# Optimization experiments

Hardware: AMD Instinct MI355X
Metric: run time of the kernel (lower is better)

## Reference

```python
import jax, jax.numpy as jnp
import numpy as np

N_NODES = 100000
N_EDGES = 1000000
DIM = 128
N_RELS = 500
N_TIMES = 1000


def setup_inputs() -> dict:
    key = jax.random.key(0)
    ks = jax.random.split(key, 8)
    h = jax.random.normal(ks[0], (N_NODES, DIM), dtype=jnp.float32)
    edge_index = jax.random.randint(ks[1], (2, N_EDGES), 0, N_NODES, dtype=jnp.int64)
    edge_type = jax.random.randint(ks[2], (N_EDGES,), 0, N_RELS, dtype=jnp.int64)
    edge_time = jax.random.randint(ks[3], (N_EDGES,), 0, N_TIMES, dtype=jnp.int64)
    query_rel = 7
    rel_table = jax.random.normal(ks[4], (N_RELS, DIM), dtype=jnp.float32)
    time_table = jax.random.normal(ks[5], (N_TIMES, DIM), dtype=jnp.float32)
    # Linear weights stored as [in, out] so y = x @ W + b
    W1 = jax.random.normal(ks[6], (4 * DIM, DIM), dtype=jnp.float32) * (1.0 / np.sqrt(4 * DIM))
    b1 = jnp.zeros((DIM,), dtype=jnp.float32)
    W2 = jax.random.normal(ks[7], (DIM, 1), dtype=jnp.float32) * (1.0 / np.sqrt(DIM))
    b2 = jnp.zeros((1,), dtype=jnp.float32)
    return {"h": h, "edge_index": edge_index, "edge_type": edge_type,
            "edge_time": edge_time, "query_rel": query_rel,
            "rel_table": rel_table, "time_table": time_table,
            "W1": W1, "b1": b1, "W2": W2, "b2": b2}


def reference(h, edge_index, edge_type, edge_time, query_rel,
              rel_table, time_table, W1, b1, W2, b2):
    src = edge_index[0]                    # [E]
    h_s = h[src]                           # [E, D] gather
    h_r = rel_table[edge_type]             # [E, D] embedding lookup
    h_t = time_table[edge_time]            # [E, D] embedding lookup
    h_rq = jnp.broadcast_to(rel_table[query_rel][None, :], h_s.shape)  # [E, D]
    x = jnp.concatenate([h_s, h_r, h_rq, h_t], axis=1)  # [E, 4D]
    hidden = jax.nn.relu(x @ W1 + b1)      # [E, D]
    alpha = hidden @ W2 + b2               # [E, 1]
    return jax.nn.sigmoid(alpha)[:, 0]     # [E]
```

## Files before the change

kernel.cpp:

```cpp
#include <hip/hip_runtime.h>
#include <hip/hip_fp16.h>
#include <hip/hip_fp8.h>
#include <math.h>

#define DIM 128

typedef _Float16 half8 __attribute__((ext_vector_type(8)));
typedef _Float16 half2v __attribute__((ext_vector_type(2)));
typedef float floatx4 __attribute__((ext_vector_type(4)));


__global__ __launch_bounds__(256) void precompute(
    const float* __restrict__ h, const float* __restrict__ rel,
    const float* __restrict__ tim, const int* __restrict__ qrel,
    const float* __restrict__ W1, const float* __restrict__ b1,
    unsigned char* __restrict__ H8, __half* __restrict__ Rh, __half* __restrict__ Th,
    int n_nodes, int n_rels, int n_times, int nHB, int nRB)
{
    const int tid = threadIdx.x;
    const int b = blockIdx.x;

    const float* A; int M, k0, row0; bool isR = false, isH = false;
    __half* Out = nullptr;
    if (b < nHB)            { A = h;   isH = true; M = n_nodes; k0 = 0;   row0 = b * 128; }
    else if (b < nHB + nRB) { A = rel; Out = Rh;   M = n_rels;  k0 = 128; row0 = (b - nHB) * 128; isR = true; }
    else                    { A = tim; Out = Th;   M = n_times; k0 = 384; row0 = (b - nHB - nRB) * 128; }

    __shared__ _Float16 fragB[32 * 64 * 8];
    __shared__ float c0f[DIM];

#pragma unroll
    for (int it = 0; it < 8; ++it) {
        const int o = tid + it * 256;
        const int ctkc = o >> 6, L = o & 63;
        const int ct = ctkc >> 2, kc = ctkc & 3;
        const int q = L >> 4, n15 = L & 15;
        const float* base = W1 + (size_t)(k0 + kc * 32 + q * 8) * DIM + ct * 16 + n15;
        half8 f;
#pragma unroll
        for (int j = 0; j < 8; ++j) f[j] = (_Float16)base[(size_t)j * DIM];
        *(half8*)&fragB[o * 8] = f;
    }
    if (isR && tid < DIM) {
        const int q = qrel[0];
        const float* hq = rel + (size_t)q * DIM;
        float s = b1[tid];
        for (int k = 0; k < DIM; ++k)
            s = fmaf(hq[k], W1[(size_t)(256 + k) * DIM + tid], s);
        c0f[tid] = s;
    }
    __syncthreads();

    const int w = tid >> 6;
    const int lane = tid & 63;
    const int m15 = lane & 15, q = lane >> 4;

    const float* aBase[2];
#pragma unroll
    for (int mt = 0; mt < 2; ++mt) {
        int arow = row0 + w * 32 + mt * 16 + m15;
        if (arow >= M) arow = M - 1;
        aBase[mt] = A + (size_t)arow * DIM + q * 8;
    }

    floatx4 acc[2][8];
#pragma unroll
    for (int mt = 0; mt < 2; ++mt)
#pragma unroll
        for (int ct = 0; ct < 8; ++ct) acc[mt][ct] = (floatx4)0.f;

#pragma unroll
    for (int kc = 0; kc < 4; ++kc) {
        half8 af[2];
#pragma unroll
        for (int mt = 0; mt < 2; ++mt) {
            const float4 a0 = *(const float4*)(aBase[mt] + kc * 32);
            const float4 a1 = *(const float4*)(aBase[mt] + kc * 32 + 4);
            af[mt][0] = (_Float16)a0.x; af[mt][1] = (_Float16)a0.y;
            af[mt][2] = (_Float16)a0.z; af[mt][3] = (_Float16)a0.w;
            af[mt][4] = (_Float16)a1.x; af[mt][5] = (_Float16)a1.y;
            af[mt][6] = (_Float16)a1.z; af[mt][7] = (_Float16)a1.w;
        }
#pragma unroll
        for (int ct = 0; ct < 8; ++ct) {
            const half8 bf = *(half8*)&fragB[(((ct * 4 + kc) * 64) + lane) * 8];
            acc[0][ct] = __builtin_amdgcn_mfma_f32_16x16x32_f16(af[0], bf, acc[0][ct], 0, 0, 0);
            acc[1][ct] = __builtin_amdgcn_mfma_f32_16x16x32_f16(af[1], bf, acc[1][ct], 0, 0, 0);
        }
    }

    float cadd[8];
#pragma unroll
    for (int ct = 0; ct < 8; ++ct) cadd[ct] = isR ? c0f[ct * 16 + m15] : 0.f;

#pragma unroll
    for (int mt = 0; mt < 2; ++mt)
#pragma unroll
        for (int r = 0; r < 4; ++r) {
            const int m = row0 + w * 32 + mt * 16 + q * 4 + r;
            if (m < M) {
                if (isH) {
                    uint2 pk;
#if __has_builtin(__builtin_amdgcn_cvt_pk_fp8_f32)
                    int w0 = 0, w1 = 0;
                    w0 = __builtin_amdgcn_cvt_pk_fp8_f32(acc[mt][0][r], acc[mt][1][r], w0, false);
                    w0 = __builtin_amdgcn_cvt_pk_fp8_f32(acc[mt][2][r], acc[mt][3][r], w0, true);
                    w1 = __builtin_amdgcn_cvt_pk_fp8_f32(acc[mt][4][r], acc[mt][5][r], w1, false);
                    w1 = __builtin_amdgcn_cvt_pk_fp8_f32(acc[mt][6][r], acc[mt][7][r], w1, true);
                    pk.x = (unsigned)w0; pk.y = (unsigned)w1;
#else
                    union { uint2 u; unsigned char bb[8]; } pu;
#pragma unroll
                    for (int ct = 0; ct < 8; ++ct)
                        pu.bb[ct] = __hip_fp8_e4m3(acc[mt][ct][r]).__x;
                    pk = pu.u;
#endif
                    *(uint2*)(H8 + (size_t)m * DIM + m15 * 8) = pk;
                } else {
                    half8 hv;
#pragma unroll
                    for (int ct = 0; ct < 8; ++ct)
                        hv[ct] = (_Float16)(acc[mt][ct][r] + cadd[ct]);
                    *(half8*)(Out + (size_t)m * DIM + m15 * 8) = hv;
                }
            }
        }
}

__device__ __forceinline__ half2v fp8x2_to_h2(unsigned u16) {
#if __has_builtin(__builtin_amdgcn_cvt_pk_f16_fp8)
    auto c = __builtin_amdgcn_cvt_pk_f16_fp8((short)u16);
    half2v r; r[0] = c[0]; r[1] = c[1];
    return r;
#else
    auto f = __builtin_amdgcn_cvt_pk_f32_fp8((int)u16, false);
    half2v r; r[0] = (_Float16)f[0]; r[1] = (_Float16)f[1];
    return r;
#endif
}

__device__ __forceinline__ float edot(uint2 hu, uint4 ru, uint4 tu,
                                      const half2v* __restrict__ w2h) {
    union U { uint4 u; half2v h[4]; };
    U R, T; R.u = ru; T.u = tu;
    const half2v z = (half2v)(_Float16)0.f;
    const unsigned hw[4] = {hu.x & 0xffffu, hu.x >> 16, hu.y & 0xffffu, hu.y >> 16};
    float p = 0.f;
#pragma unroll
    for (int j = 0; j < 4; ++j) {
        const half2v hh = fp8x2_to_h2(hw[j]);
        half2v s = hh + R.h[j] + T.h[j];
        s = __builtin_elementwise_max(s, z);
#if __has_builtin(__builtin_amdgcn_fdot2)
        p = __builtin_amdgcn_fdot2(s, w2h[j], p, false);
#else
        p = fmaf((float)s[0], (float)w2h[j][0], p);
        p = fmaf((float)s[1], (float)w2h[j][1], p);
#endif
    }
    return p;
}

__global__ __launch_bounds__(256) void edge_kernel(
    const int* __restrict__ ei, const int* __restrict__ ety,
    const int* __restrict__ eti,
    const unsigned char* __restrict__ H8, const __half* __restrict__ Rh,
    const __half* __restrict__ Th,
    const float* __restrict__ W2, const float* __restrict__ b2,
    float* __restrict__ out, int E, int nGrpTotal)
{
    const int tid = threadIdx.x;
    const int l = tid & 15;
    int g = blockIdx.x * 16 + (tid >> 4);
    const int nQuad = (E + 3) >> 2;
    if (g >= nQuad) return;

    half2v w2h[4];
#pragma unroll
    for (int j = 0; j < 4; ++j) {
        w2h[j][0] = (_Float16)W2[(2 * j) * 16 + l];
        w2h[j][1] = (_Float16)W2[(2 * j + 1) * 16 + l];
    }
    const float b2v = b2[0];
    const bool exact = (E & 3) == 0;

    int s[4], r[4], t[4];
    {
        const int e0 = 4 * g;
        if (exact || e0 + 3 < E) {
#pragma unroll
            for (int i = 0; i < 4; ++i) { s[i] = ei[e0 + i]; r[i] = ety[e0 + i]; t[i] = eti[e0 + i]; }
        } else {
#pragma unroll
            for (int i = 0; i < 4; ++i) {
                const int e = min(e0 + i, E - 1);
                s[i] = ei[e]; r[i] = ety[e]; t[i] = eti[e];
            }
        }
    }

    while (true) {
        const int gn = g + nGrpTotal;
        uint2 hv[4]; uint4 rv[4], tv[4];
#pragma unroll
        for (int i = 0; i < 4; ++i) {
            hv[i] = ((const uint2*)(H8 + (size_t)s[i] * DIM))[l];
            rv[i] = ((const uint4*)(Rh + (size_t)r[i] * DIM))[l];
            tv[i] = ((const uint4*)(Th + (size_t)t[i] * DIM))[l];
        }
        if (gn < nQuad) {
            const int e0 = 4 * gn;
            if (exact || e0 + 3 < E) {
#pragma unroll
                for (int i = 0; i < 4; ++i) { s[i] = ei[e0 + i]; r[i] = ety[e0 + i]; t[i] = eti[e0 + i]; }
            } else {
#pragma unroll
                for (int i = 0; i < 4; ++i) {
                    const int e = min(e0 + i, E - 1);
                    s[i] = ei[e]; r[i] = ety[e]; t[i] = eti[e];
                }
            }
        }
        float p[4];
#pragma unroll
        for (int i = 0; i < 4; ++i)
            p[i] = edot(hv[i], rv[i], tv[i], w2h);
#pragma unroll
        for (int off = 8; off > 0; off >>= 1) {
#pragma unroll
            for (int i = 0; i < 4; ++i)
                p[i] += __shfl_down(p[i], off, 16);
        }
        if (l == 0) {
            const int e0 = 4 * g;
            float4 o;
            o.x = 1.f / (1.f + __expf(-(p[0] + b2v)));
            o.y = 1.f / (1.f + __expf(-(p[1] + b2v)));
            o.z = 1.f / (1.f + __expf(-(p[2] + b2v)));
            o.w = 1.f / (1.f + __expf(-(p[3] + b2v)));
            if (e0 + 3 < E) {
                *(float4*)(out + e0) = o;
            } else {
                const float ov[4] = {o.x, o.y, o.z, o.w};
                for (int i = 0; i < 4 && e0 + i < E; ++i) out[e0 + i] = ov[i];
            }
        }
        if (gn >= nQuad) break;
        g = gn;
    }
}

extern "C" void kernel_launch(void* const* d_in, const int* in_sizes, int n_in,
                              void* d_out, int out_size, void* d_ws, size_t ws_size,
                              hipStream_t stream) {
    const float* h          = (const float*)d_in[0];
    const int*   edge_index = (const int*)d_in[1];
    const int*   edge_type  = (const int*)d_in[2];
    const int*   edge_time  = (const int*)d_in[3];
    const int*   query_rel  = (const int*)d_in[4];
    const float* rel_table  = (const float*)d_in[5];
    const float* time_table = (const float*)d_in[6];
    const float* W1         = (const float*)d_in[7];
    const float* b1         = (const float*)d_in[8];
    const float* W2         = (const float*)d_in[9];
    const float* b2         = (const float*)d_in[10];
    float* out = (float*)d_out;

    const int n_nodes = in_sizes[0] / DIM;
    const int E       = in_sizes[2];
    const int n_rels  = in_sizes[5] / DIM;
    const int n_times = in_sizes[6] / DIM;

    unsigned char* H8 = (unsigned char*)d_ws;
    __half* Rh = (__half*)(H8 + (((size_t)n_nodes * DIM + 255) & ~(size_t)255));
    __half* Th = Rh + (size_t)n_rels * DIM;

    const int nHB = (n_nodes + 127) / 128;
    const int nRB = (n_rels + 127) / 128;
    const int nTB = (n_times + 127) / 128;

    precompute<<<nHB + nRB + nTB, 256, 0, stream>>>(
        h, rel_table, time_table, query_rel, W1, b1,
        H8, Rh, Th, n_nodes, n_rels, n_times, nHB, nRB);

    const int nBlk = 4096;
    edge_kernel<<<nBlk, 256, 0, stream>>>(
        edge_index, edge_type, edge_time, H8, Rh, Th, W2, b2,
        out, E, nBlk * 16);
}
```

Measured before the change: 157.3 us.

## Process one edge per 8-lane group with 16-byte fp8 loads

Restructures the edge kernel so each 8-lane group handles a single edge, with each lane loading 16 fp8 H values and 16 half values each from the relation and time tables, instead of 16-lane groups handling four edges at a time. This shortens the shuffle reduction to three steps and widens the per-lane gathers. In exchange it gives up the four-edge batching that kept multiple gathers in flight per lane and the vectorized float4 output stores. The W2 lane mapping is remapped to match the new element layout.

```diff
diff --git a/kernel.cpp b/kernel.cpp
--- a/kernel.cpp
+++ b/kernel.cpp
@@ -139,17 +139,20 @@
 #endif
 }
 
-__device__ __forceinline__ float edot(uint2 hu, uint4 ru, uint4 tu,
-                                      const half2v* __restrict__ w2h) {
+__device__ __forceinline__ float edot16(uint4 hu, uint4 r0, uint4 r1,
+                                        uint4 t0, uint4 t1,
+                                        const half2v* __restrict__ w2h) {
     union U { uint4 u; half2v h[4]; };
-    U R, T; R.u = ru; T.u = tu;
+    U R0, R1, T0, T1; R0.u = r0; R1.u = r1; T0.u = t0; T1.u = t1;
     const half2v z = (half2v)(_Float16)0.f;
-    const unsigned hw[4] = {hu.x & 0xffffu, hu.x >> 16, hu.y & 0xffffu, hu.y >> 16};
+    const unsigned hw[8] = {hu.x & 0xffffu, hu.x >> 16, hu.y & 0xffffu, hu.y >> 16,
+                            hu.z & 0xffffu, hu.z >> 16, hu.w & 0xffffu, hu.w >> 16};
     float p = 0.f;
 #pragma unroll
-    for (int j = 0; j < 4; ++j) {
-        const half2v hh = fp8x2_to_h2(hw[j]);
-        half2v s = hh + R.h[j] + T.h[j];
+    for (int j = 0; j < 8; ++j) {
+        const half2v rr = (j < 4) ? R0.h[j] : R1.h[j - 4];
+        const half2v tt = (j < 4) ? T0.h[j] : T1.h[j - 4];
+        half2v s = fp8x2_to_h2(hw[j]) + rr + tt;
         s = __builtin_elementwise_max(s, z);
 #if __has_builtin(__builtin_amdgcn_fdot2)
         p = __builtin_amdgcn_fdot2(s, w2h[j], p, false);
@@ -170,83 +173,42 @@
     float* __restrict__ out, int E, int nGrpTotal)
 {
     const int tid = threadIdx.x;
-    const int l = tid & 15;
-    int g = blockIdx.x * 16 + (tid >> 4);
-    const int nQuad = (E + 3) >> 2;
-    if (g >= nQuad) return;
-
-    half2v w2h[4];
+    const int l = tid & 7;
+    int e = blockIdx.x * 32 + (tid >> 3);
+    if (e >= E) return;
+
+    half2v w2h[8];
 #pragma unroll
     for (int j = 0; j < 4; ++j) {
-        w2h[j][0] = (_Float16)W2[(2 * j) * 16 + l];
-        w2h[j][1] = (_Float16)W2[(2 * j + 1) * 16 + l];
+        w2h[j][0]     = (_Float16)W2[32 * j + 2 * l];
+        w2h[j][1]     = (_Float16)W2[32 * j + 16 + 2 * l];
+        w2h[j + 4][0] = (_Float16)W2[32 * j + 2 * l + 1];
+        w2h[j + 4][1] = (_Float16)W2[32 * j + 16 + 2 * l + 1];
     }
     const float b2v = b2[0];
-    const bool exact = (E & 3) == 0;
-
-    int s[4], r[4], t[4];
-    {
-        const int e0 = 4 * g;
-        if (exact || e0 + 3 < E) {
-#pragma unroll
-            for (int i = 0; i < 4; ++i) { s[i] = ei[e0 + i]; r[i] = ety[e0 + i]; t[i] = eti[e0 + i]; }
-        } else {
-#pragma unroll
-            for (int i = 0; i < 4; ++i) {
-                const int e = min(e0 + i, E - 1);
-                s[i] = ei[e]; r[i] = ety[e]; t[i] = eti[e];
-            }
-        }
-    }
+    const int stride = nGrpTotal;
+
+    int s = ei[e], r = ety[e], t = eti[e];
 
     while (true) {
-        const int gn = g + nGrpTotal;
-        uint2 hv[4]; uint4 rv[4], tv[4];
-#pragma unroll
-        for (int i = 0; i < 4; ++i) {
-            hv[i] = ((const uint2*)(H8 + (size_t)s[i] * DIM))[l];
-            rv[i] = ((const uint4*)(Rh + (size_t)r[i] * DIM))[l];
-            tv[i] = ((const uint4*)(Th + (size_t)t[i] * DIM))[l];
-        }
-        if (gn < nQuad) {
-            const int e0 = 4 * gn;
-            if (exact || e0 + 3 < E) {
-#pragma unroll
-                for (int i = 0; i < 4; ++i) { s[i] = ei[e0 + i]; r[i] = ety[e0 + i]; t[i] = eti[e0 + i]; }
-            } else {
-#pragma unroll
-                for (int i = 0; i < 4; ++i) {
-                    const int e = min(e0 + i, E - 1);
-                    s[i] = ei[e]; r[i] = ety[e]; t[i] = eti[e];
-                }
-            }
-        }
-        float p[4];
-#pragma unroll
-        for (int i = 0; i < 4; ++i)
-            p[i] = edot(hv[i], rv[i], tv[i], w2h);
-#pragma unroll
-        for (int off = 8; off > 0; off >>= 1) {
-#pragma unroll
-            for (int i = 0; i < 4; ++i)
-                p[i] += __shfl_down(p[i], off, 16);
-        }
-        if (l == 0) {
-            const int e0 = 4 * g;
-            float4 o;
-            o.x = 1.f / (1.f + __expf(-(p[0] + b2v)));
-            o.y = 1.f / (1.f + __expf(-(p[1] + b2v)));
-            o.z = 1.f / (1.f + __expf(-(p[2] + b2v)));
-            o.w = 1.f / (1.f + __expf(-(p[3] + b2v)));
-            if (e0 + 3 < E) {
-                *(float4*)(out + e0) = o;
-            } else {
-                const float ov[4] = {o.x, o.y, o.z, o.w};
-                for (int i = 0; i < 4 && e0 + i < E; ++i) out[e0 + i] = ov[i];
-            }
-        }
-        if (gn >= nQuad) break;
-        g = gn;
+        const int en = e + stride;
+        const uint4* hp = (const uint4*)(H8 + (size_t)s * DIM);
+        const uint4* rp = (const uint4*)(Rh + (size_t)r * DIM);
+        const uint4* tp = (const uint4*)(Th + (size_t)t * DIM);
+        const uint4 hv  = hp[l];
+        const uint4 rv0 = rp[2 * l], rv1 = rp[2 * l + 1];
+        const uint4 tv0 = tp[2 * l], tv1 = tp[2 * l + 1];
+        if (en < E) {
+            s = ei[en]; r = ety[en]; t = eti[en];
+        }
+        float p = edot16(hv, rv0, rv1, tv0, tv1, w2h);
+        p += __shfl_down(p, 4, 8);
+        p += __shfl_down(p, 2, 8);
+        p += __shfl_down(p, 1, 8);
+        if (l == 0)
+            out[e] = 1.f / (1.f + __expf(-(p + b2v)));
+        if (en >= E) break;
+        e = en;
     }
 }
 
@@ -286,5 +248,5 @@
     const int nBlk = 4096;
     edge_kernel<<<nBlk, 256, 0, stream>>>(
         edge_index, edge_type, edge_time, H8, Rh, Th, W2, b2,
-        out, E, nBlk * 16);
-}
+        out, E, nBlk * 32);
+}
```

Result: no change. 159.2 us (+1.2%).
